# Kernel optimization log

Measured on AMD Instinct MI355X. Metric: run time of the kernel, lower is better.

## Reference

```python
import jax, jax.numpy as jnp
import numpy as np

N = 100000
SEQ = 12
DIMS = [32, 64, 64, 32]


def _glorot(key, shape):
    fan_in, fan_out = shape[0], shape[1]
    lim = jnp.sqrt(6.0 / (fan_in + fan_out))
    return jax.random.uniform(key, shape, jnp.float32, -lim, lim)


def setup_inputs() -> dict:
    key = jax.random.key(0)
    ks = jax.random.split(key, 8)
    x = jax.random.normal(ks[0], (N, DIMS[0], 1), dtype=jnp.float32)
    spiral_indices = jax.random.randint(ks[1], (N, SEQ), 0, N)
    # SpiralConv i: Linear(SEQ * DIMS[i], DIMS[i+1])
    W0 = _glorot(ks[2], (SEQ * DIMS[0], DIMS[1]))
    b0 = jnp.zeros((DIMS[1],), jnp.float32)
    W1 = _glorot(ks[3], (SEQ * DIMS[1], DIMS[2]))
    b1 = jnp.zeros((DIMS[2],), jnp.float32)
    W2 = _glorot(ks[4], (SEQ * DIMS[2], DIMS[3]))
    b2 = jnp.zeros((DIMS[3],), jnp.float32)
    return {"x": x, "spiral_indices": spiral_indices,
            "W0": W0, "b0": b0, "W1": W1, "b1": b1, "W2": W2, "b2": b2}


def _spiral_conv(h, idx, W, b):
    # h: [N, C]; idx: [N, SEQ] -> gathered [N, SEQ, C] -> flat [N, SEQ*C]
    n = h.shape[0]
    g = jnp.take(h, idx, axis=0).reshape(n, -1)
    return g @ W + b


def reference(x, spiral_indices, W0, b0, W1, b1, W2, b2):
    h = x[..., 0]  # squeeze(-1): [N, C_in]
    h = jax.nn.elu(_spiral_conv(h, spiral_indices, W0, b0))
    h = jax.nn.elu(_spiral_conv(h, spiral_indices, W1, b1))
    h = _spiral_conv(h, spiral_indices, W2, b2)  # final_activation=False
    return h[:, :, None]
```

## Files before the change

kernel.cpp:

```cpp
#include <hip/hip_runtime.h>
#include <math.h>


typedef __bf16 bf16;
typedef bf16  bf16x4 __attribute__((ext_vector_type(4)));
typedef bf16  bf16x8 __attribute__((ext_vector_type(8)));
typedef float f32x4  __attribute__((ext_vector_type(4)));

template<int CIN, int COUT>
__device__ inline void pack_one(const float* __restrict__ W, bf16* __restrict__ BP, int e) {
    constexpr int NT = COUT / 16, CC = CIN / 32;
    const int f = e >> 9, r = e & 511, lane = r >> 3, j = r & 7;
    const int t = f % NT, cc = (f / NT) % CC, s = f / (NT * CC);
    const int col = t * 16 + (lane & 15);
    const int k   = s * CIN + cc * 32 + (lane >> 4) * 8 + j;
    BP[e] = (bf16)W[k * COUT + col];
}

__global__ __launch_bounds__(256)
void prep_all(const float* __restrict__ x, bf16* __restrict__ xb,
              const float* __restrict__ W0, const float* __restrict__ W1,
              const float* __restrict__ W2, bf16* __restrict__ B0,
              bf16* __restrict__ B1, bf16* __restrict__ B2, int n)
{
    const int gid = blockIdx.x * 256 + threadIdx.x;
    const int e = gid * 4;
    if (e < n * 32) {
        const f32x4 v = *reinterpret_cast<const f32x4*>(x + e);
        bf16x4 o = {(bf16)v[0], (bf16)v[1], (bf16)v[2], (bf16)v[3]};
        *reinterpret_cast<bf16x4*>(xb + e) = o;
    }
    if (gid < 384 * 64)                       pack_one<32, 64>(W0, B0, gid);
    else if (gid < 384 * 64 + 768 * 64)       pack_one<64, 64>(W1, B1, gid - 384 * 64);
    else if (gid < 384 * 64 + 768 * 64 + 768 * 32)
                                              pack_one<64, 32>(W2, B2, gid - 384 * 64 - 768 * 64);
}

template<int CIN, int COUT, bool ELU, typename TOUT>
__global__ __launch_bounds__(256, 5)
void spiral_mfma(const bf16* __restrict__ h, const int* __restrict__ idx,
                 const bf16* __restrict__ BP, const float* __restrict__ bias,
                 TOUT* __restrict__ out, int n)
{
    constexpr int CC  = CIN / 32;
    constexpr int NT  = COUT / 16;
    constexpr int PS  = CIN * COUT;
    constexpr int SC  = 6 / CC;
    constexpr int NCH = 12 / SC;
    constexpr int PL  = 6;

    __shared__ bf16 Bs[SC * PS];

    const int tid  = threadIdx.x;
    const int lane = tid & 63;
    const int wave = tid >> 6;
    const int m    = lane & 15;
    const int quad = lane >> 4;
    const int i0   = (blockIdx.x * 4 + wave) * 16;
    const bool valid = (i0 < n);

    const int ir = min(i0 + m, n - 1);
    const int4* ip = reinterpret_cast<const int4*>(idx + (size_t)ir * 12);
    const int4 q0 = ip[0], q1 = ip[1], q2 = ip[2];
    const int rg[12] = {q0.x,q0.y,q0.z,q0.w, q1.x,q1.y,q1.z,q1.w, q2.x,q2.y,q2.z,q2.w};

    f32x4 acc[NT] = {};

    #pragma unroll
    for (int c = 0; c < NCH; ++c) {
        if (c) __syncthreads();
        const bf16* src = BP + (size_t)c * SC * PS;
        #pragma unroll
        for (int r2 = tid; r2 < SC * PS / 8; r2 += 256)
            *reinterpret_cast<bf16x8*>(&Bs[r2 * 8]) =
                *reinterpret_cast<const bf16x8*>(&src[r2 * 8]);
        __syncthreads();

        bf16x8 a[PL];
        #pragma unroll
        for (int sl = 0; sl < SC; ++sl)
            #pragma unroll
            for (int cc = 0; cc < CC; ++cc)
                a[sl * CC + cc] = *reinterpret_cast<const bf16x8*>(
                    h + (size_t)rg[c * SC + sl] * CIN + cc * 32 + quad * 8);
        __builtin_amdgcn_sched_barrier(0);
        #pragma unroll
        for (int p = 0; p < PL; ++p)
            #pragma unroll
            for (int t = 0; t < NT; ++t) {
                const bf16x8 b = *reinterpret_cast<const bf16x8*>(
                    &Bs[(p * NT + t) * 512 + lane * 8]);
                acc[t] = __builtin_amdgcn_mfma_f32_16x16x32_bf16(a[p], b, acc[t], 0, 0, 0);
            }
    }

    if (!valid) return;

    #pragma unroll
    for (int t = 0; t < NT; ++t) {
        const int col = t * 16 + m;
        const float bv = bias[col];
        #pragma unroll
        for (int g = 0; g < 4; ++g) {
            const int row = i0 + quad * 4 + g;
            float v = acc[t][g] + bv;
            if (ELU) v = (v > 0.f) ? v : (__expf(v) - 1.f);
            out[(size_t)row * COUT + col] = (TOUT)v;
        }
    }
}

extern "C" void kernel_launch(void* const* d_in, const int* in_sizes, int n_in,
                              void* d_out, int out_size, void* d_ws, size_t ws_size,
                              hipStream_t stream) {
    const float* x   = (const float*)d_in[0];
    const int*   idx = (const int*)d_in[1];
    const float* W0  = (const float*)d_in[2];
    const float* b0  = (const float*)d_in[3];
    const float* W1  = (const float*)d_in[4];
    const float* b1  = (const float*)d_in[5];
    const float* W2  = (const float*)d_in[6];
    const float* b2  = (const float*)d_in[7];
    float* out = (float*)d_out;

    const int n = in_sizes[0] / 32;

    bf16* xb = (bf16*)d_ws;
    bf16* h1 = xb + (size_t)n * 32;
    bf16* h2 = h1 + (size_t)n * 64;
    bf16* B0 = h2 + (size_t)n * 64;
    bf16* B1 = B0 + 384 * 64;
    bf16* B2 = B1 + 768 * 64;

    const int prep_threads = n * 8;
    prep_all<<<(prep_threads + 255) / 256, dim3(256), 0, stream>>>(x, xb, W0, W1, W2, B0, B1, B2, n);

    const int grid = (n + 63) / 64;
    spiral_mfma<32, 64, true,  bf16 ><<<grid, dim3(256), 0, stream>>>(xb, idx, B0, b0, h1,  n);
    spiral_mfma<64, 64, true,  bf16 ><<<grid, dim3(256), 0, stream>>>(h1, idx, B1, b1, h2,  n);
    spiral_mfma<64, 32, false, float><<<grid, dim3(256), 0, stream>>>(h2, idx, B2, b2, out, n);
}
```

Baseline: 158.9 us.

## Split 64-channel activations into two 32-channel planes and add nontemporal memory ops

Stores the 64-channel hidden activations as two separate 32-channel half-planes, each with 64-byte rows. Gathers for layers 2 and 3 then run in two phases, so each phase reads one compact plane and hits fewer cache lines per neighbour. Weight packing is reordered to match the phase/spiral order. Index loads and output stores become nontemporal hints, which may help or hurt cache reuse, since the indices are read again by each of the three layers.

```diff
diff --git a/kernel.cpp b/kernel.cpp
--- a/kernel.cpp
+++ b/kernel.cpp
@@ -6,14 +6,15 @@
 typedef bf16  bf16x4 __attribute__((ext_vector_type(4)));
 typedef bf16  bf16x8 __attribute__((ext_vector_type(8)));
 typedef float f32x4  __attribute__((ext_vector_type(4)));
+typedef int   intx4  __attribute__((ext_vector_type(4)));
 
 template<int CIN, int COUT>
 __device__ inline void pack_one(const float* __restrict__ W, bf16* __restrict__ BP, int e) {
-    constexpr int NT = COUT / 16, CC = CIN / 32;
+    constexpr int NT = COUT / 16;
     const int f = e >> 9, r = e & 511, lane = r >> 3, j = r & 7;
-    const int t = f % NT, cc = (f / NT) % CC, s = f / (NT * CC);
+    const int t = f % NT, s = (f / NT) % 12, ph = f / (NT * 12);
     const int col = t * 16 + (lane & 15);
-    const int k   = s * CIN + cc * 32 + (lane >> 4) * 8 + j;
+    const int k   = s * CIN + ph * 32 + (lane >> 4) * 8 + j;
     BP[e] = (bf16)W[k * COUT + col];
 }
 
@@ -36,20 +37,18 @@
                                               pack_one<64, 32>(W2, B2, gid - 384 * 64 - 768 * 64);
 }
 
-template<int CIN, int COUT, bool ELU, typename TOUT>
+template<int PH, int COUT, bool ELU, bool SPLITOUT, typename TOUT>
 __global__ __launch_bounds__(256, 5)
-void spiral_mfma(const bf16* __restrict__ h, const int* __restrict__ idx,
-                 const bf16* __restrict__ BP, const float* __restrict__ bias,
-                 TOUT* __restrict__ out, int n)
+void spiral_mfma(const bf16* __restrict__ hA, const bf16* __restrict__ hB,
+                 const int* __restrict__ idx, const bf16* __restrict__ BP,
+                 const float* __restrict__ bias,
+                 TOUT* __restrict__ outA, TOUT* __restrict__ outB, int n)
 {
-    constexpr int CC  = CIN / 32;
     constexpr int NT  = COUT / 16;
-    constexpr int PS  = CIN * COUT;
-    constexpr int SC  = 6 / CC;
-    constexpr int NCH = 12 / SC;
-    constexpr int PL  = 6;
+    constexpr int NCH = 2 * PH;
+    constexpr int CHE = 6 * 32 * COUT;
 
-    __shared__ bf16 Bs[SC * PS];
+    __shared__ bf16 Bs[CHE];
 
     const int tid  = threadIdx.x;
     const int lane = tid & 63;
@@ -60,8 +59,10 @@
     const bool valid = (i0 < n);
 
     const int ir = min(i0 + m, n - 1);
-    const int4* ip = reinterpret_cast<const int4*>(idx + (size_t)ir * 12);
-    const int4 q0 = ip[0], q1 = ip[1], q2 = ip[2];
+    const intx4* ip = reinterpret_cast<const intx4*>(idx + (size_t)ir * 12);
+    const intx4 q0 = __builtin_nontemporal_load(ip);
+    const intx4 q1 = __builtin_nontemporal_load(ip + 1);
+    const intx4 q2 = __builtin_nontemporal_load(ip + 2);
     const int rg[12] = {q0.x,q0.y,q0.z,q0.w, q1.x,q1.y,q1.z,q1.w, q2.x,q2.y,q2.z,q2.w};
 
     f32x4 acc[NT] = {};
@@ -69,23 +70,25 @@
     #pragma unroll
     for (int c = 0; c < NCH; ++c) {
         if (c) __syncthreads();
-        const bf16* src = BP + (size_t)c * SC * PS;
+        const bf16* src = BP + (size_t)c * CHE;
         #pragma unroll
-        for (int r2 = tid; r2 < SC * PS / 8; r2 += 256)
+        for (int r2 = tid; r2 < CHE / 8; r2 += 256)
             *reinterpret_cast<bf16x8*>(&Bs[r2 * 8]) =
                 *reinterpret_cast<const bf16x8*>(&src[r2 * 8]);
         __syncthreads();
 
-        bf16x8 a[PL];
+        const int ph = (PH == 2) ? (c >> 1) : 0;
+        const int sb = (PH == 2) ? ((c & 1) * 6) : (c * 6);
+        const bf16* tab = ph ? hB : hA;
+
+        bf16x8 a[6];
         #pragma unroll
-        for (int sl = 0; sl < SC; ++sl)
-            #pragma unroll
-            for (int cc = 0; cc < CC; ++cc)
-                a[sl * CC + cc] = *reinterpret_cast<const bf16x8*>(
-                    h + (size_t)rg[c * SC + sl] * CIN + cc * 32 + quad * 8);
+        for (int sl = 0; sl < 6; ++sl)
+            a[sl] = *reinterpret_cast<const bf16x8*>(
+                tab + (size_t)rg[sb + sl] * 32 + quad * 8);
         __builtin_amdgcn_sched_barrier(0);
         #pragma unroll
-        for (int p = 0; p < PL; ++p)
+        for (int p = 0; p < 6; ++p)
             #pragma unroll
             for (int t = 0; t < NT; ++t) {
                 const bf16x8 b = *reinterpret_cast<const bf16x8*>(
@@ -105,7 +108,12 @@
             const int row = i0 + quad * 4 + g;
             float v = acc[t][g] + bv;
             if (ELU) v = (v > 0.f) ? v : (__expf(v) - 1.f);
-            out[(size_t)row * COUT + col] = (TOUT)v;
+            if (SPLITOUT) {
+                TOUT* o = (t < 2) ? outA : outB;
+                __builtin_nontemporal_store((TOUT)v, o + (size_t)row * 32 + (t & 1) * 16 + m);
+            } else {
+                __builtin_nontemporal_store((TOUT)v, outA + (size_t)row * COUT + col);
+            }
         }
     }
 }
@@ -125,18 +133,20 @@
 
     const int n = in_sizes[0] / 32;
 
-    bf16* xb = (bf16*)d_ws;
-    bf16* h1 = xb + (size_t)n * 32;
-    bf16* h2 = h1 + (size_t)n * 64;
-    bf16* B0 = h2 + (size_t)n * 64;
-    bf16* B1 = B0 + 384 * 64;
-    bf16* B2 = B1 + 768 * 64;
+    bf16* xb  = (bf16*)d_ws;
+    bf16* h1A = xb  + (size_t)n * 32;
+    bf16* h1B = h1A + (size_t)n * 32;
+    bf16* h2A = h1B + (size_t)n * 32;
+    bf16* h2B = h2A + (size_t)n * 32;
+    bf16* B0  = h2B + (size_t)n * 32;
+    bf16* B1  = B0 + 384 * 64;
+    bf16* B2  = B1 + 768 * 64;
 
     const int prep_threads = n * 8;
     prep_all<<<(prep_threads + 255) / 256, dim3(256), 0, stream>>>(x, xb, W0, W1, W2, B0, B1, B2, n);
 
     const int grid = (n + 63) / 64;
-    spiral_mfma<32, 64, true,  bf16 ><<<grid, dim3(256), 0, stream>>>(xb, idx, B0, b0, h1,  n);
-    spiral_mfma<64, 64, true,  bf16 ><<<grid, dim3(256), 0, stream>>>(h1, idx, B1, b1, h2,  n);
-    spiral_mfma<64, 32, false, float><<<grid, dim3(256), 0, stream>>>(h2, idx, B2, b2, out, n);
+    spiral_mfma<1, 64, true,  true,  bf16 ><<<grid, dim3(256), 0, stream>>>(xb,  nullptr, idx, B0, b0, h1A, h1B, n);
+    spiral_mfma<2, 64, true,  true,  bf16 ><<<grid, dim3(256), 0, stream>>>(h1A, h1B,     idx, B1, b1, h2A, h2B, n);
+    spiral_mfma<2, 32, false, false, float><<<grid, dim3(256), 0, stream>>>(h2A, h2B,     idx, B2, b2, out, nullptr, n);
 }
```

Result: slower. 170.4 us (+7.2%).

## Quantize intermediate activations to int8 with per-row scales to shrink gathers

Applied to the files above, without the earlier changes.

Layer outputs h1 and h2 are now stored as int8 with a per-row float scale, computed by a max reduction across the 16-lane row group, instead of bf16. The next layer gathers 8-byte int8 chunks plus the scales and dequantizes to bf16 before the MFMA. This halves the bytes moved by the random-index neighbor gathers. The cost is extra ALU for dequantization and reduction, an extra scattered scale load per neighbor, and a real loss of accuracy versus bf16 that may exceed tolerance. The final float output also switches to nontemporal stores.

```diff
diff --git a/kernel.cpp b/kernel.cpp
--- a/kernel.cpp
+++ b/kernel.cpp
@@ -36,11 +36,12 @@
                                               pack_one<64, 32>(W2, B2, gid - 384 * 64 - 768 * 64);
 }
 
-template<int CIN, int COUT, bool ELU, typename TOUT>
+template<int CIN, int COUT, bool ELU, int AMODE, int OMODE, typename TOUT>
 __global__ __launch_bounds__(256, 5)
-void spiral_mfma(const bf16* __restrict__ h, const int* __restrict__ idx,
-                 const bf16* __restrict__ BP, const float* __restrict__ bias,
-                 TOUT* __restrict__ out, int n)
+void spiral_mfma(const void* __restrict__ hin, const float* __restrict__ scin,
+                 const int* __restrict__ idx, const bf16* __restrict__ BP,
+                 const float* __restrict__ bias,
+                 TOUT* __restrict__ out, float* __restrict__ scout, int n)
 {
     constexpr int CC  = CIN / 32;
     constexpr int NT  = COUT / 16;
@@ -64,6 +65,12 @@
     const int4 q0 = ip[0], q1 = ip[1], q2 = ip[2];
     const int rg[12] = {q0.x,q0.y,q0.z,q0.w, q1.x,q1.y,q1.z,q1.w, q2.x,q2.y,q2.z,q2.w};
 
+    float sc[12];
+    if (AMODE == 1) {
+        #pragma unroll
+        for (int s = 0; s < 12; ++s) sc[s] = scin[rg[s]];
+    }
+
     f32x4 acc[NT] = {};
 
     #pragma unroll
@@ -77,13 +84,41 @@
         __syncthreads();
 
         bf16x8 a[PL];
-        #pragma unroll
-        for (int sl = 0; sl < SC; ++sl)
-            #pragma unroll
-            for (int cc = 0; cc < CC; ++cc)
-                a[sl * CC + cc] = *reinterpret_cast<const bf16x8*>(
-                    h + (size_t)rg[c * SC + sl] * CIN + cc * 32 + quad * 8);
-        __builtin_amdgcn_sched_barrier(0);
+        if (AMODE == 0) {
+            const bf16* h = (const bf16*)hin;
+            #pragma unroll
+            for (int sl = 0; sl < SC; ++sl)
+                #pragma unroll
+                for (int cc = 0; cc < CC; ++cc)
+                    a[sl * CC + cc] = *reinterpret_cast<const bf16x8*>(
+                        h + (size_t)rg[c * SC + sl] * CIN + cc * 32 + quad * 8);
+            __builtin_amdgcn_sched_barrier(0);
+        } else {
+            const signed char* h = (const signed char*)hin;
+            int2 raw[PL];
+            #pragma unroll
+            for (int sl = 0; sl < SC; ++sl)
+                #pragma unroll
+                for (int cc = 0; cc < CC; ++cc)
+                    raw[sl * CC + cc] = *reinterpret_cast<const int2*>(
+                        h + (size_t)rg[c * SC + sl] * CIN + cc * 32 + quad * 8);
+            __builtin_amdgcn_sched_barrier(0);
+            #pragma unroll
+            for (int sl = 0; sl < SC; ++sl) {
+                const float scl = sc[c * SC + sl];
+                #pragma unroll
+                for (int cc = 0; cc < CC; ++cc) {
+                    const int2 r = raw[sl * CC + cc];
+                    bf16x8 av;
+                    #pragma unroll
+                    for (int j = 0; j < 4; ++j) {
+                        av[j]     = (bf16)((float)((signed char)((r.x >> (8 * j)) & 0xff)) * scl);
+                        av[j + 4] = (bf16)((float)((signed char)((r.y >> (8 * j)) & 0xff)) * scl);
+                    }
+                    a[sl * CC + cc] = av;
+                }
+            }
+        }
         #pragma unroll
         for (int p = 0; p < PL; ++p)
             #pragma unroll
@@ -96,16 +131,42 @@
 
     if (!valid) return;
 
+    float v[NT][4];
     #pragma unroll
     for (int t = 0; t < NT; ++t) {
-        const int col = t * 16 + m;
-        const float bv = bias[col];
+        const float bv = bias[t * 16 + m];
         #pragma unroll
         for (int g = 0; g < 4; ++g) {
+            float x = acc[t][g] + bv;
+            if (ELU) x = (x > 0.f) ? x : (__expf(x) - 1.f);
+            v[t][g] = x;
+        }
+    }
+
+    if (OMODE == 2) {
+        #pragma unroll
+        for (int t = 0; t < NT; ++t)
+            #pragma unroll
+            for (int g = 0; g < 4; ++g)
+                __builtin_nontemporal_store((TOUT)v[t][g],
+                    out + (size_t)(i0 + quad * 4 + g) * COUT + t * 16 + m);
+    } else {
+        #pragma unroll
+        for (int g = 0; g < 4; ++g) {
+            float mx = 0.f;
+            #pragma unroll
+            for (int t = 0; t < NT; ++t) mx = fmaxf(mx, fabsf(v[t][g]));
+            #pragma unroll
+            for (int d = 1; d < 16; d <<= 1)
+                mx = fmaxf(mx, __shfl_xor(mx, d, 16));
+            const float qs = (mx > 0.f) ? 127.f / mx : 0.f;
             const int row = i0 + quad * 4 + g;
-            float v = acc[t][g] + bv;
-            if (ELU) v = (v > 0.f) ? v : (__expf(v) - 1.f);
-            out[(size_t)row * COUT + col] = (TOUT)v;
+            #pragma unroll
+            for (int t = 0; t < NT; ++t) {
+                const int q = (int)rintf(v[t][g] * qs);
+                out[(size_t)row * COUT + t * 16 + m] = (TOUT)q;
+            }
+            if (m == 0) scout[row] = (mx > 0.f) ? mx / 127.f : 0.f;
         }
     }
 }
@@ -125,18 +186,23 @@
 
     const int n = in_sizes[0] / 32;
 
-    bf16* xb = (bf16*)d_ws;
-    bf16* h1 = xb + (size_t)n * 32;
-    bf16* h2 = h1 + (size_t)n * 64;
-    bf16* B0 = h2 + (size_t)n * 64;
-    bf16* B1 = B0 + 384 * 64;
-    bf16* B2 = B1 + 768 * 64;
+    bf16*        xb = (bf16*)d_ws;
+    signed char* h1 = (signed char*)(xb + (size_t)n * 32);
+    signed char* h2 = h1 + (size_t)n * 64;
+    float*       s1 = (float*)(h2 + (size_t)n * 64);
+    float*       s2 = s1 + n;
+    bf16*        B0 = (bf16*)(s2 + n);
+    bf16*        B1 = B0 + 384 * 64;
+    bf16*        B2 = B1 + 768 * 64;
 
     const int prep_threads = n * 8;
     prep_all<<<(prep_threads + 255) / 256, dim3(256), 0, stream>>>(x, xb, W0, W1, W2, B0, B1, B2, n);
 
     const int grid = (n + 63) / 64;
-    spiral_mfma<32, 64, true,  bf16 ><<<grid, dim3(256), 0, stream>>>(xb, idx, B0, b0, h1,  n);
-    spiral_mfma<64, 64, true,  bf16 ><<<grid, dim3(256), 0, stream>>>(h1, idx, B1, b1, h2,  n);
-    spiral_mfma<64, 32, false, float><<<grid, dim3(256), 0, stream>>>(h2, idx, B2, b2, out, n);
-}
+    spiral_mfma<32, 64, true,  0, 1, signed char><<<grid, dim3(256), 0, stream>>>(
+        xb, nullptr, idx, B0, b0, h1, s1, n);
+    spiral_mfma<64, 64, true,  1, 1, signed char><<<grid, dim3(256), 0, stream>>>(
+        h1, s1, idx, B1, b1, h2, s2, n);
+    spiral_mfma<64, 32, false, 1, 2, float      ><<<grid, dim3(256), 0, stream>>>(
+        h2, s2, idx, B2, b2, out, nullptr, n);
+}
```

After: 166.1 us. 4.6% more time.
